# Kernel tuning notes

Hardware: AMD Instinct MI355X
Metric: run time of the kernel (lower is better)

## Reference

```python
import jax, jax.numpy as jnp
import numpy as np

V, BLK, D, H, L = 50257, 2048, 768, 12, 4
HD = D // H
EPS = 1e-5


def _ln(x, w, b):
    mu = jnp.mean(x, axis=-1, keepdims=True)
    var = jnp.mean(jnp.square(x - mu), axis=-1, keepdims=True)
    return (x - mu) * jax.lax.rsqrt(var + EPS) * w + b


def setup_inputs() -> dict:
    key = jax.random.key(0)
    ks = iter(jax.random.split(key, 32))
    s = 0.02
    idx = jax.random.randint(next(ks), (2, 2048), 0, V)
    inp = {
        "idx": idx,
        "wte": jax.random.normal(next(ks), (V, D), jnp.float32) * s,
        "wpe": jax.random.normal(next(ks), (BLK, D), jnp.float32) * s,
        # stacked per-layer params [L, ...]
        "ln1_w": jnp.ones((L, D), jnp.float32),
        "ln1_b": jnp.zeros((L, D), jnp.float32),
        "attn_w": jax.random.normal(next(ks), (L, D, 3 * D), jnp.float32) * s,
        "attn_b": jnp.zeros((L, 3 * D), jnp.float32),
        "proj_w": jax.random.normal(next(ks), (L, D, D), jnp.float32) * (s / np.sqrt(2 * L)),
        "proj_b": jnp.zeros((L, D), jnp.float32),
        "ln2_w": jnp.ones((L, D), jnp.float32),
        "ln2_b": jnp.zeros((L, D), jnp.float32),
        "fc_w": jax.random.normal(next(ks), (L, D, 4 * D), jnp.float32) * s,
        "fc_b": jnp.zeros((L, 4 * D), jnp.float32),
        "fcp_w": jax.random.normal(next(ks), (L, 4 * D, D), jnp.float32) * (s / np.sqrt(2 * L)),
        "fcp_b": jnp.zeros((L, D), jnp.float32),
        "lnf_w": jnp.ones((D,), jnp.float32),
        "lnf_b": jnp.zeros((D,), jnp.float32),
    }
    return inp


def _gpt_forward(idx, wte, wpe, ln1_w, ln1_b, attn_w, attn_b, proj_w, proj_b,
                 ln2_w, ln2_b, fc_w, fc_b, fcp_w, fcp_b, lnf_w, lnf_b):
    B, T = idx.shape
    x = wte[idx] + wpe[:T]  # [B,T,D]; dropout p=0 -> identity
    causal = jnp.tril(jnp.ones((T, T), bool))
    scale = 1.0 / np.sqrt(HD)

    def block(x, p):
        l1w, l1b, aw, ab, pw, pb, l2w, l2b, fw, fb, fpw, fpb = p
        h = _ln(x, l1w, l1b)
        qkv = h @ aw + ab  # [B,T,3D]
        q, k, v = jnp.split(qkv, 3, axis=-1)
        q = q.reshape(B, T, H, HD).transpose(0, 2, 1, 3)  # [B,H,T,hd]
        k = k.reshape(B, T, H, HD).transpose(0, 2, 1, 3)
        v = v.reshape(B, T, H, HD).transpose(0, 2, 1, 3)
        att = jnp.einsum('bhqd,bhkd->bhqk', q, k) * scale
        att = jnp.where(causal, att, -jnp.inf)
        att = jax.nn.softmax(att, axis=-1)
        y = jnp.einsum('bhqk,bhkd->bhqd', att, v)
        y = y.transpose(0, 2, 1, 3).reshape(B, T, D)
        x = x + y @ pw + pb
        h2 = _ln(x, l2w, l2b)
        m = jax.nn.gelu(h2 @ fw + fb, approximate=False) @ fpw + fpb
        return x + m, None

    params = (ln1_w, ln1_b, attn_w, attn_b, proj_w, proj_b,
              ln2_w, ln2_b, fc_w, fc_b, fcp_w, fcp_b)
    x, _ = jax.lax.scan(block, x, params)
    x = _ln(x, lnf_w, lnf_b)
    # inference path: logits only for last position, lm_head tied to wte
    logits = x[:, -1:, :] @ wte.T  # [B,1,V]
    return logits


def reference(idx, wte, wpe, ln1_w, ln1_b, attn_w, attn_b, proj_w, proj_b,
              ln2_w, ln2_b, fc_w, fc_b, fcp_w, fcp_b, lnf_w, lnf_b):
    return _gpt_forward(idx, wte, wpe, ln1_w, ln1_b, attn_w, attn_b, proj_w, proj_b,
                        ln2_w, ln2_b, fc_w, fc_b, fcp_w, fcp_b, lnf_w, lnf_b)
```

## Files before the change

kernel.cpp:

```cpp
#include <hip/hip_runtime.h>
#include <math.h>

#define V 50257
#define B 2
#define T 2048
#define D 768
#define H 12
#define HD 64
#define L 4
#define D3 (3*D)
#define D4 (4*D)
#define NTOK (B*T)
#define EPS 1e-5f

typedef __bf16 v8bf __attribute__((ext_vector_type(8)));
typedef __bf16 v4bf __attribute__((ext_vector_type(4)));
typedef unsigned short v8us __attribute__((ext_vector_type(8)));
typedef float  v4f  __attribute__((ext_vector_type(4)));

#define GAS(p) ((const __attribute__((address_space(1))) void*)(p))
#define LAS(p) ((__attribute__((address_space(3))) void*)(p))

#define LIDX(row, chunk) ((row)*64 + ((((chunk) ^ ((row)&7)))<<3))
#define CIDX(row, chunk) ((row)*128 + ((((chunk) ^ ((row)&7)))<<3))

#define SBAR() asm volatile("s_barrier" ::: "memory")

__global__ __launch_bounds__(256) void prep_kernel(
        const int* __restrict__ idx, const float* __restrict__ wte,
        const float* __restrict__ wpe, float* __restrict__ x,
        const float* __restrict__ aw_all,  const float* __restrict__ pw_all,
        const float* __restrict__ fw_all,  const float* __restrict__ fpw_all,
        __bf16* __restrict__ awt_all, __bf16* __restrict__ pwt_all,
        __bf16* __restrict__ fwt_all, __bf16* __restrict__ fpwt_all) {
    int bid = blockIdx.x;
    if (bid < 3072) {
        int e = (bid * 256 + threadIdx.x) * 4;
        int pos = e / D;
        int d   = e - pos * D;
        int t   = pos & (T - 1);
        int tok = idx[pos];
        const float4 a  = *(const float4*)(wte + (size_t)tok * D + d);
        const float4 p4 = *(const float4*)(wpe + (size_t)t * D + d);
        float4 r; r.x = a.x + p4.x; r.y = a.y + p4.y; r.z = a.z + p4.z; r.w = a.w + p4.w;
        *(float4*)(x + e) = r;
        return;
    }
    bid -= 3072;
    const int l = bid / 6912; bid -= l * 6912;
    const float* W; __bf16* Wt; int K, N, bx, by;
    if (bid < 1728)      {             W = aw_all  + (size_t)l * D  * D3; Wt = awt_all  + (size_t)l * D3 * D;  K = D;  N = D3; bx = bid % 72; by = bid / 72; }
    else if (bid < 2304) { bid -= 1728; W = pw_all  + (size_t)l * D  * D;  Wt = pwt_all  + (size_t)l * D  * D;  K = D;  N = D;  bx = bid % 24; by = bid / 24; }
    else if (bid < 4608) { bid -= 2304; W = fw_all  + (size_t)l * D  * D4; Wt = fwt_all  + (size_t)l * D4 * D;  K = D;  N = D4; bx = bid % 96; by = bid / 96; }
    else                 { bid -= 4608; W = fpw_all + (size_t)l * D4 * D;  Wt = fpwt_all + (size_t)l * D  * D4; K = D4; N = D;  bx = bid % 24; by = bid / 24; }
    __shared__ float t[32][33];
    const int n0 = bx * 32, k0 = by * 32;
    const int tx = threadIdx.x & 31, ty = threadIdx.x >> 5;
    #pragma unroll
    for (int p = 0; p < 4; ++p)
        t[ty + 8 * p][tx] = W[(size_t)(k0 + ty + 8 * p) * N + n0 + tx];
    __syncthreads();
    #pragma unroll
    for (int p = 0; p < 4; ++p)
        Wt[(size_t)(n0 + ty + 8 * p) * K + k0 + tx] = (__bf16)t[tx][ty + 8 * p];
}

__global__ __launch_bounds__(256) void ln_kernel(const float* __restrict__ X,
                                                 const float* __restrict__ w,
                                                 const float* __restrict__ b,
                                                 __bf16* __restrict__ Y,
                                                 int src_mul, int src_off) {
    int srow = blockIdx.x * src_mul + src_off;
    const float* xr = X + (size_t)srow * D;
    float v[3];
    float s = 0.f, s2 = 0.f;
    #pragma unroll
    for (int j = 0; j < 3; ++j) {
        v[j] = xr[threadIdx.x + 256 * j];
        s += v[j];
        s2 += v[j] * v[j];
    }
    #pragma unroll
    for (int off = 32; off; off >>= 1) {
        s  += __shfl_xor(s, off);
        s2 += __shfl_xor(s2, off);
    }
    __shared__ float ss[4], ss2[4];
    int wave = threadIdx.x >> 6, lane = threadIdx.x & 63;
    if (lane == 0) { ss[wave] = s; ss2[wave] = s2; }
    __syncthreads();
    s  = ss[0] + ss[1] + ss[2] + ss[3];
    s2 = ss2[0] + ss2[1] + ss2[2] + ss2[3];
    float mu  = s * (1.f / D);
    float var = s2 * (1.f / D) - mu * mu;
    float rs  = rsqrtf(var + EPS);
    __bf16* yr = Y + (size_t)blockIdx.x * D;
    #pragma unroll
    for (int j = 0; j < 3; ++j) {
        int c = threadIdx.x + 256 * j;
        yr[c] = (__bf16)((v[j] - mu) * rs * w[c] + b[c]);
    }
}

template<bool DOGELU>
__global__ __launch_bounds__(256) void gemm_bt(const __bf16* __restrict__ A,
                                               const __bf16* __restrict__ Wt,
                                               const float* __restrict__ bias,
                                               __bf16* __restrict__ Cout,
                                               int N, int K) {
    __shared__ __align__(16) __bf16 sm[24576];
    const int tid  = threadIdx.x;
    const int w    = tid >> 6;
    const int lane = tid & 63;

    int fid = blockIdx.y * gridDim.x + blockIdx.x;
    const int nwg = gridDim.x * gridDim.y;
    fid = (fid & 7) * (nwg >> 3) + (fid >> 3);
    const int row0 = (fid / gridDim.x) * 128;
    const int col0 = (fid % gridDim.x) * 128;

    const int srow = ((tid >> 6) & 3) * 16 + (tid & 15);
    const int sk   = ((tid >> 4) & 3) * 8;
    const __bf16* gA0 = A  + (size_t)(row0 + srow) * K + sk;
    const __bf16* gA1 = gA0 + (size_t)64 * K;
    const __bf16* gB0 = Wt + (size_t)(col0 + srow) * K + sk;
    const __bf16* gB1 = gB0 + (size_t)64 * K;

    auto stage = [&](int bsel) {
        __bf16* dst = sm + bsel * 8192;
        __builtin_amdgcn_global_load_lds(GAS(gA0), LAS(dst + (size_t)tid * 8), 16, 0, 0);
        __builtin_amdgcn_global_load_lds(GAS(gA1), LAS(dst + (size_t)(tid + 256) * 8), 16, 0, 0);
        __builtin_amdgcn_global_load_lds(GAS(gB0), LAS(dst + 4096 + (size_t)tid * 8), 16, 0, 0);
        __builtin_amdgcn_global_load_lds(GAS(gB1), LAS(dst + 4096 + (size_t)(tid + 256) * 8), 16, 0, 0);
        gA0 += 32; gA1 += 32; gB0 += 32; gB1 += 32;
    };

    const int wr = w >> 1, wc = w & 1;
    const __bf16* rA = sm + wr * 2048 + lane * 8;
    const __bf16* rB = sm + 4096 + wc * 2048 + lane * 8;

    const int nt = K >> 5;
    stage(0); stage(1);

    v4f acc[4][4] = {};
    for (int t = 0; t < nt; ++t) {
        const int cb = (t % 3) * 8192;
        if (t + 2 < nt) {
            stage((t + 2) % 3);
            asm volatile("s_waitcnt vmcnt(8)\n\ts_barrier" ::: "memory");
        } else if (t + 1 < nt) {
            asm volatile("s_waitcnt vmcnt(4)\n\ts_barrier" ::: "memory");
        } else {
            asm volatile("s_waitcnt vmcnt(0)\n\ts_barrier" ::: "memory");
        }
        v8bf af[4], bfr[4];
        #pragma unroll
        for (int i = 0; i < 4; ++i) af[i]  = *(const v8bf*)(rA + cb + i * 512);
        #pragma unroll
        for (int j = 0; j < 4; ++j) bfr[j] = *(const v8bf*)(rB + cb + j * 512);
        #pragma unroll
        for (int i = 0; i < 4; ++i)
            #pragma unroll
            for (int j = 0; j < 4; ++j)
                acc[i][j] = __builtin_amdgcn_mfma_f32_16x16x32_bf16(af[i], bfr[j], acc[i][j], 0, 0, 0);
        SBAR();
    }

    const int er = (lane >> 4) * 4;
    const int ec = lane & 15;
    #pragma unroll
    for (int j = 0; j < 4; ++j) {
        const int col = wc * 64 + j * 16 + ec;
        const float bval = bias[col0 + col];
        const int chunk = col >> 3, ce = col & 7;
        #pragma unroll
        for (int i = 0; i < 4; ++i) {
            const int rowb = wr * 64 + i * 16 + er;
            #pragma unroll
            for (int rr = 0; rr < 4; ++rr) {
                float vv = acc[i][j][rr] + bval;
                if (DOGELU) vv = 0.5f * vv * (1.f + erff(vv * 0.70710678118f));
                sm[CIDX(rowb + rr, chunk) + ce] = (__bf16)vv;
            }
        }
    }
    __syncthreads();
    #pragma unroll
    for (int c = 0; c < 8; ++c) {
        const int chunkid = tid + c * 256;
        const int row = chunkid >> 4;
        const int cc  = chunkid & 15;
        *(v8us*)(void*)(Cout + (size_t)(row0 + row) * N + col0 + cc * 8) =
            *(const v8us*)(const void*)(sm + CIDX(row, cc));
    }
}

__global__ __launch_bounds__(256) void gemm64(const __bf16* __restrict__ A,
                                              const __bf16* __restrict__ Wt,
                                              const float* __restrict__ bias,
                                              const float* __restrict__ res,
                                              float* __restrict__ Cout,
                                              int N, int K) {
    __shared__ __align__(16) __bf16 sm[24576];
    const int tid  = threadIdx.x;
    const int w    = tid >> 6;
    const int lane = tid & 63;

    int fid = blockIdx.y * gridDim.x + blockIdx.x;
    const int nwg = gridDim.x * gridDim.y;
    fid = (fid & 7) * (nwg >> 3) + (fid >> 3);
    const int row0 = (fid / gridDim.x) * 64;
    const int col0 = (fid % gridDim.x) * 64;

    const int srow = ((tid >> 7) & 3) * 16 + (tid & 15);
    const int sk   = ((tid >> 4) & 7) * 8;
    const __bf16* gA0 = A  + (size_t)(row0 + srow) * K + sk;
    const __bf16* gA1 = gA0 + (size_t)32 * K;
    const __bf16* gB0 = Wt + (size_t)(col0 + srow) * K + sk;
    const __bf16* gB1 = gB0 + (size_t)32 * K;

    auto stage = [&](int bsel) {
        __bf16* dst = sm + bsel * 8192;
        __builtin_amdgcn_global_load_lds(GAS(gA0), LAS(dst + (size_t)tid * 8), 16, 0, 0);
        __builtin_amdgcn_global_load_lds(GAS(gA1), LAS(dst + (size_t)(tid + 256) * 8), 16, 0, 0);
        __builtin_amdgcn_global_load_lds(GAS(gB0), LAS(dst + 4096 + (size_t)tid * 8), 16, 0, 0);
        __builtin_amdgcn_global_load_lds(GAS(gB1), LAS(dst + 4096 + (size_t)(tid + 256) * 8), 16, 0, 0);
        gA0 += 64; gA1 += 64; gB0 += 64; gB1 += 64;
    };

    const int wr = w >> 1, wc = w & 1;
    const __bf16* rA = sm + wr * 2048 + lane * 8;
    const __bf16* rB = sm + 4096 + wc * 2048 + lane * 8;

    const int nt = K >> 6;
    stage(0); stage(1);

    v4f acc[2][2] = {};
    for (int t = 0; t < nt; ++t) {
        const int cb = (t % 3) * 8192;
        if (t + 2 < nt) {
            stage((t + 2) % 3);
            asm volatile("s_waitcnt vmcnt(8)\n\ts_barrier" ::: "memory");
        } else if (t + 1 < nt) {
            asm volatile("s_waitcnt vmcnt(4)\n\ts_barrier" ::: "memory");
        } else {
            asm volatile("s_waitcnt vmcnt(0)\n\ts_barrier" ::: "memory");
        }
        #pragma unroll
        for (int h = 0; h < 2; ++h) {
            v8bf af[2], bfr[2];
            #pragma unroll
            for (int i = 0; i < 2; ++i) af[i]  = *(const v8bf*)(rA + cb + i * 1024 + h * 512);
            #pragma unroll
            for (int j = 0; j < 2; ++j) bfr[j] = *(const v8bf*)(rB + cb + j * 1024 + h * 512);
            #pragma unroll
            for (int i = 0; i < 2; ++i)
                #pragma unroll
                for (int j = 0; j < 2; ++j)
                    acc[i][j] = __builtin_amdgcn_mfma_f32_16x16x32_bf16(af[i], bfr[j], acc[i][j], 0, 0, 0);
        }
        SBAR();
    }

    float* smf = (float*)sm;
    const int er = (lane >> 4) * 4;
    const int ec = lane & 15;
    #pragma unroll
    for (int j = 0; j < 2; ++j) {
        const int col = wc * 32 + j * 16 + ec;
        const float bval = bias[col0 + col];
        #pragma unroll
        for (int i = 0; i < 2; ++i) {
            #pragma unroll
            for (int rr = 0; rr < 4; ++rr) {
                const int row = wr * 32 + i * 16 + er + rr;
                smf[row * 64 + (col ^ ((row & 3) << 4))] = acc[i][j][rr] + bval;
            }
        }
    }
    __syncthreads();
    #pragma unroll
    for (int c = 0; c < 4; ++c) {
        const int chunkid = tid + c * 256;
        const int row = chunkid >> 4;
        const int c0  = (chunkid & 15) * 4;
        float4 vv = *(const float4*)(smf + row * 64 + (c0 ^ ((row & 3) << 4)));
        const float4 rv = *(const float4*)(res + (size_t)(row0 + row) * N + col0 + c0);
        vv.x += rv.x; vv.y += rv.y; vv.z += rv.z; vv.w += rv.w;
        *(float4*)(Cout + (size_t)(row0 + row) * N + col0 + c0) = vv;
    }
}

__global__ __launch_bounds__(256) void attn_mfma(const __bf16* __restrict__ qkv,
                                                 __bf16* __restrict__ y) {
    __shared__ __align__(16) __bf16 Qs[4096];
    __shared__ __align__(16) __bf16 Ks[4096];
    __shared__ __align__(16) __bf16 Vt[4096];
    __shared__ __align__(16) __bf16 Ps[4][1024];

    const int tid  = threadIdx.x;
    const int w    = tid >> 6;
    const int lane = tid & 63;
    const int quad = lane >> 4;
    const int l4   = lane & 15;

    int fid = blockIdx.x;
    const int nwg = gridDim.x;
    fid = (fid & 7) * (nwg >> 3) + (fid >> 3);

    const int qt = 31 - (fid & 31);
    const int bh = fid >> 5;
    const int b  = bh / H;
    const int h  = bh - b * H;
    const int q0 = qt * 64;

    const __bf16* base = qkv + (size_t)(b * T) * D3 + h * HD;

    {
        int c = tid;
        #pragma unroll
        for (int rep = 0; rep < 2; ++rep, c += 256) {
            int row = c >> 3, ch = c & 7;
            v8us v = *(const v8us*)(const void*)(base + (size_t)(q0 + row) * D3 + ch * 8);
            *(v8us*)(void*)(Qs + LIDX(row, ch)) = v;
        }
    }

    const int krow = tid >> 3, kch = tid & 7;
    const int vkp = tid & 31, vdc = tid >> 5;
    const __bf16* kp0 = base + D     + (size_t)krow * D3 + kch * 8;
    const __bf16* kp1 = kp0 + (size_t)32 * D3;
    const __bf16* vp0 = base + 2 * D + (size_t)(2 * vkp) * D3 + vdc * 8;
    const __bf16* vp1 = vp0 + D3;

    v8us kr0 = *(const v8us*)(const void*)kp0;
    v8us kr1 = *(const v8us*)(const void*)kp1;
    v8us vr0 = *(const v8us*)(const void*)vp0;
    v8us vr1 = *(const v8us*)(const void*)vp1;

    float m_local = -INFINITY;
    v4f o[4] = {};
    v4f sacc = {};
    v8bf qf[2];
    v8bf vones;
    #pragma unroll
    for (int i = 0; i < 8; ++i) vones[i] = (__bf16)1.0f;

    const int nt = qt + 1;
    const size_t adv = (size_t)64 * D3;
    const int qrow = q0 + w * 16 + l4;

    for (int kt = 0; kt < nt; ++kt) {
        const int k0 = kt * 64;
        *(v8us*)(void*)(Ks + LIDX(krow, kch))      = kr0;
        *(v8us*)(void*)(Ks + LIDX(krow + 32, kch)) = kr1;
        #pragma unroll
        for (int j = 0; j < 8; ++j) {
            int dim = vdc * 8 + j;
            int idx = dim * 64 + ((((vkp >> 2) ^ (dim & 7))) << 3) + ((vkp & 3) << 1);
            *(unsigned int*)(void*)(Vt + idx) =
                ((unsigned int)vr1[j] << 16) | (unsigned int)vr0[j];
        }
        __syncthreads();

        if (kt == 0) {
            #pragma unroll
            for (int kh = 0; kh < 2; ++kh)
                qf[kh] = *(const v8bf*)(Qs + LIDX(w * 16 + l4, kh * 4 + quad));
        }
        if (kt + 1 < nt) {
            kp0 += adv; kp1 += adv; vp0 += adv; vp1 += adv;
            kr0 = *(const v8us*)(const void*)kp0;
            kr1 = *(const v8us*)(const void*)kp1;
            vr0 = *(const v8us*)(const void*)vp0;
            vr1 = *(const v8us*)(const void*)vp1;
        }

        v4f s[4] = {};
        __builtin_amdgcn_s_setprio(1);
        #pragma unroll
        for (int kh = 0; kh < 2; ++kh) {
            #pragma unroll
            for (int jb = 0; jb < 4; ++jb) {
                v8bf bk = *(const v8bf*)(Ks + LIDX(jb * 16 + l4, kh * 4 + quad));
                s[jb] = __builtin_amdgcn_mfma_f32_16x16x32_bf16(bk, qf[kh], s[jb], 0, 0, 0);
            }
        }
        __builtin_amdgcn_s_setprio(0);

        float sv[4][4];
        float mx = -INFINITY;
        #pragma unroll
        for (int jb = 0; jb < 4; ++jb) {
            #pragma unroll
            for (int rg = 0; rg < 4; ++rg) {
                float vvv = s[jb][rg] * 0.125f;
                if (k0 + jb * 16 + quad * 4 + rg > qrow) vvv = -INFINITY;
                sv[jb][rg] = vvv;
                mx = fmaxf(mx, vvv);
            }
        }
        mx = fmaxf(mx, __shfl_xor(mx, 16));
        mx = fmaxf(mx, __shfl_xor(mx, 32));
        if (!__all(mx <= m_local + 8.f)) {
            const float mnew    = fmaxf(m_local, mx);
            const float alpha_l = __expf(m_local - mnew);
            m_local = mnew;
            float a4[4];
            #pragma unroll
            for (int r = 0; r < 4; ++r) a4[r] = __shfl(alpha_l, quad * 4 + r);
            #pragma unroll
            for (int r = 0; r < 4; ++r) {
                sacc[r] *= a4[r];
                #pragma unroll
                for (int db = 0; db < 4; ++db) o[db][r] *= a4[r];
            }
        }
        #pragma unroll
        for (int jb = 0; jb < 4; ++jb) {
            v4bf pk;
            #pragma unroll
            for (int rg = 0; rg < 4; ++rg)
                pk[rg] = (__bf16)__expf(sv[jb][rg] - m_local);
            *(v4bf*)(void*)(&Ps[w][LIDX(l4, jb * 2 + (quad >> 1)) + ((quad & 1) << 2)]) = pk;
        }
        __builtin_amdgcn_s_setprio(1);
        #pragma unroll
        for (int kh = 0; kh < 2; ++kh) {
            v8bf ap = *(const v8bf*)(&Ps[w][LIDX(l4, kh * 4 + quad)]);
            sacc = __builtin_amdgcn_mfma_f32_16x16x32_bf16(ap, vones, sacc, 0, 0, 0);
            #pragma unroll
            for (int db = 0; db < 4; ++db) {
                v8bf bv = *(const v8bf*)(Vt + LIDX(db * 16 + l4, kh * 4 + quad));
                o[db] = __builtin_amdgcn_mfma_f32_16x16x32_bf16(ap, bv, o[db], 0, 0, 0);
            }
        }
        __builtin_amdgcn_s_setprio(0);
        __syncthreads();
    }

    #pragma unroll
    for (int db = 0; db < 4; ++db) {
        #pragma unroll
        for (int r = 0; r < 4; ++r) {
            const int q = q0 + w * 16 + quad * 4 + r;
            y[(size_t)(b * T + q) * D + h * HD + db * 16 + l4] =
                (__bf16)(o[db][r] / sacc[r]);
        }
    }
}

__global__ __launch_bounds__(256) void logits_kernel(const __bf16* __restrict__ xf,
                                                     const float* __restrict__ wte,
                                                     float* __restrict__ out) {
    int wave = threadIdx.x >> 6;
    int lane = threadIdx.x & 63;
    int v = blockIdx.x * 4 + wave;
    if (v >= V) return;
    const float4* wr = (const float4*)(wte + (size_t)v * D);
    const v4bf*   x0 = (const v4bf*)(xf);
    const v4bf*   x1 = (const v4bf*)(xf + D);
    float s0 = 0.f, s1 = 0.f;
    #pragma unroll
    for (int j = 0; j < 3; ++j) {
        float4 wv = wr[lane + 64 * j];
        v4bf a0 = x0[lane + 64 * j];
        v4bf a1 = x1[lane + 64 * j];
        s0 = fmaf(wv.x, (float)a0[0], s0); s0 = fmaf(wv.y, (float)a0[1], s0);
        s0 = fmaf(wv.z, (float)a0[2], s0); s0 = fmaf(wv.w, (float)a0[3], s0);
        s1 = fmaf(wv.x, (float)a1[0], s1); s1 = fmaf(wv.y, (float)a1[1], s1);
        s1 = fmaf(wv.z, (float)a1[2], s1); s1 = fmaf(wv.w, (float)a1[3], s1);
    }
    #pragma unroll
    for (int off = 32; off; off >>= 1) {
        s0 += __shfl_xor(s0, off);
        s1 += __shfl_xor(s1, off);
    }
    if (lane == 0) { out[v] = s0; out[V + v] = s1; }
}

extern "C" void kernel_launch(void* const* d_in, const int* in_sizes, int n_in,
                              void* d_out, int out_size, void* d_ws, size_t ws_size,
                              hipStream_t stream) {
    const int*   idx    = (const int*)  d_in[0];
    const float* wte    = (const float*)d_in[1];
    const float* wpe    = (const float*)d_in[2];
    const float* ln1_w  = (const float*)d_in[3];
    const float* ln1_b  = (const float*)d_in[4];
    const float* attn_w = (const float*)d_in[5];
    const float* attn_b = (const float*)d_in[6];
    const float* proj_w = (const float*)d_in[7];
    const float* proj_b = (const float*)d_in[8];
    const float* ln2_w  = (const float*)d_in[9];
    const float* ln2_b  = (const float*)d_in[10];
    const float* fc_w   = (const float*)d_in[11];
    const float* fc_b   = (const float*)d_in[12];
    const float* fcp_w  = (const float*)d_in[13];
    const float* fcp_b  = (const float*)d_in[14];
    const float* lnf_w  = (const float*)d_in[15];
    const float* lnf_b  = (const float*)d_in[16];
    float* out = (float*)d_out;

    char* ws = (char*)d_ws;
    float*  x    = (float*)ws;  ws += (size_t)NTOK * D  * 4;
    __bf16* qkvb = (__bf16*)ws;
    __bf16* gb   = (__bf16*)ws; ws += (size_t)NTOK * D4 * 2;
    __bf16* hb   = (__bf16*)ws; ws += (size_t)NTOK * D  * 2;
    __bf16* yb   = (__bf16*)ws; ws += (size_t)NTOK * D  * 2;
    __bf16* awt  = (__bf16*)ws; ws += (size_t)L * D3 * D   * 2;
    __bf16* pwt  = (__bf16*)ws; ws += (size_t)L * D  * D   * 2;
    __bf16* fwt  = (__bf16*)ws; ws += (size_t)L * D4 * D   * 2;
    __bf16* fpwt = (__bf16*)ws; ws += (size_t)L * D  * D4  * 2;
    __bf16* xf   = (__bf16*)ws; ws += (size_t)B * D    * 2;

    prep_kernel<<<3072 + 6912 * L, 256, 0, stream>>>(idx, wte, wpe, x,
                                                     attn_w, proj_w, fc_w, fcp_w,
                                                     awt, pwt, fwt, fpwt);

    for (int l = 0; l < L; ++l) {
        const float* l1w = ln1_w + l * D;
        const float* l1b = ln1_b + l * D;
        const float* ab  = attn_b + l * D3;
        const float* pb  = proj_b + l * D;
        const float* l2w = ln2_w + l * D;
        const float* l2b = ln2_b + l * D;
        const float* fb  = fc_b + l * D4;
        const float* fpb = fcp_b + l * D;
        const __bf16* awl  = awt  + (size_t)l * D3 * D;
        const __bf16* pwl  = pwt  + (size_t)l * D  * D;
        const __bf16* fwl  = fwt  + (size_t)l * D4 * D;
        const __bf16* fpwl = fpwt + (size_t)l * D  * D4;

        ln_kernel<<<NTOK, 256, 0, stream>>>(x, l1w, l1b, hb, 1, 0);
        gemm_bt<false><<<dim3(D3 / 128, NTOK / 128), 256, 0, stream>>>(
            hb, awl, ab, qkvb, D3, D);
        attn_mfma<<<B * H * (T / 64), 256, 0, stream>>>(qkvb, yb);
        gemm64<<<dim3(D / 64, NTOK / 64), 256, 0, stream>>>(
            yb, pwl, pb, x, x, D, D);
        ln_kernel<<<NTOK, 256, 0, stream>>>(x, l2w, l2b, hb, 1, 0);
        gemm_bt<true><<<dim3(D4 / 128, NTOK / 128), 256, 0, stream>>>(
            hb, fwl, fb, gb, D4, D);
        gemm64<<<dim3(D / 64, NTOK / 64), 256, 0, stream>>>(
            gb, fpwl, fpb, x, x, D, D4);
    }

    ln_kernel<<<B, 256, 0, stream>>>(x, lnf_w, lnf_b, xf, T, T - 1);
    logits_kernel<<<(V + 3) / 4, 256, 0, stream>>>(xf, wte, out);
}
```

Measured before the change: 1.265 ms.

## Double-buffer K/V tiles in attention and use polynomial erf for GELU

The attention kernel now keeps two LDS buffers for the K and V tiles, so it writes the next tile while the current one is consumed, and it needs one barrier per iteration instead of two. The goal is to overlap LDS staging with the MFMA and softmax work and to cut synchronization. The FC GELU epilogue also swaps erff for an Abramowitz-Stegun polynomial erf approximation with about 1e-7 error, which lowers epilogue ALU cost at a small accuracy risk. LDS use rises by 16 KB per block, which may reduce occupancy.

Result: no change. 1.251 ms (-1.1%).

```diff
diff --git a/kernel.cpp b/kernel.cpp
--- a/kernel.cpp
+++ b/kernel.cpp
@@ -25,6 +25,16 @@
 #define CIDX(row, chunk) ((row)*128 + ((((chunk) ^ ((row)&7)))<<3))
 
 #define SBAR() asm volatile("s_barrier" ::: "memory")
+
+__device__ __forceinline__ float gelu_fast(float x) {
+    float z  = fabsf(x) * 0.70710678118f;
+    float tt = 1.f / (1.f + 0.3275911f * z);
+    float poly = tt * (0.254829592f + tt * (-0.284496736f + tt * (1.421413741f +
+                 tt * (-1.453152027f + tt * 1.061405429f))));
+    float er = 1.f - poly * __expf(-z * z);
+    er = (x < 0.f) ? -er : er;
+    return 0.5f * x * (1.f + er);
+}
 
 __global__ __launch_bounds__(256) void prep_kernel(
         const int* __restrict__ idx, const float* __restrict__ wte,
@@ -179,7 +189,7 @@
             #pragma unroll
             for (int rr = 0; rr < 4; ++rr) {
                 float vv = acc[i][j][rr] + bval;
-                if (DOGELU) vv = 0.5f * vv * (1.f + erff(vv * 0.70710678118f));
+                if (DOGELU) vv = gelu_fast(vv);
                 sm[CIDX(rowb + rr, chunk) + ce] = (__bf16)vv;
             }
         }
@@ -294,8 +304,8 @@
 __global__ __launch_bounds__(256) void attn_mfma(const __bf16* __restrict__ qkv,
                                                  __bf16* __restrict__ y) {
     __shared__ __align__(16) __bf16 Qs[4096];
-    __shared__ __align__(16) __bf16 Ks[4096];
-    __shared__ __align__(16) __bf16 Vt[4096];
+    __shared__ __align__(16) __bf16 Ks[8192];
+    __shared__ __align__(16) __bf16 Vt[8192];
     __shared__ __align__(16) __bf16 Ps[4][1024];
 
     const int tid  = threadIdx.x;
@@ -338,43 +348,45 @@
     v8us vr0 = *(const v8us*)(const void*)vp0;
     v8us vr1 = *(const v8us*)(const void*)vp1;
 
+    const int nt = qt + 1;
+    const size_t adv = (size_t)64 * D3;
+
+    *(v8us*)(void*)(Ks + LIDX(krow, kch))      = kr0;
+    *(v8us*)(void*)(Ks + LIDX(krow + 32, kch)) = kr1;
+    #pragma unroll
+    for (int j = 0; j < 8; ++j) {
+        int dim = vdc * 8 + j;
+        int idx = dim * 64 + ((((vkp >> 2) ^ (dim & 7))) << 3) + ((vkp & 3) << 1);
+        *(unsigned int*)(void*)(Vt + idx) =
+            ((unsigned int)vr1[j] << 16) | (unsigned int)vr0[j];
+    }
+    if (nt > 1) {
+        kp0 += adv; kp1 += adv; vp0 += adv; vp1 += adv;
+        kr0 = *(const v8us*)(const void*)kp0;
+        kr1 = *(const v8us*)(const void*)kp1;
+        vr0 = *(const v8us*)(const void*)vp0;
+        vr1 = *(const v8us*)(const void*)vp1;
+    }
+    __syncthreads();
+
+    v8bf qf[2];
+    #pragma unroll
+    for (int kh = 0; kh < 2; ++kh)
+        qf[kh] = *(const v8bf*)(Qs + LIDX(w * 16 + l4, kh * 4 + quad));
+
     float m_local = -INFINITY;
     v4f o[4] = {};
     v4f sacc = {};
-    v8bf qf[2];
     v8bf vones;
     #pragma unroll
     for (int i = 0; i < 8; ++i) vones[i] = (__bf16)1.0f;
 
-    const int nt = qt + 1;
-    const size_t adv = (size_t)64 * D3;
     const int qrow = q0 + w * 16 + l4;
 
     for (int kt = 0; kt < nt; ++kt) {
+        const int cur = (kt & 1) << 12;
+        const int nxt = cur ^ 4096;
         const int k0 = kt * 64;
-        *(v8us*)(void*)(Ks + LIDX(krow, kch))      = kr0;
-        *(v8us*)(void*)(Ks + LIDX(krow + 32, kch)) = kr1;
-        #pragma unroll
-        for (int j = 0; j < 8; ++j) {
-            int dim = vdc * 8 + j;
-            int idx = dim * 64 + ((((vkp >> 2) ^ (dim & 7))) << 3) + ((vkp & 3) << 1);
-            *(unsigned int*)(void*)(Vt + idx) =
-                ((unsigned int)vr1[j] << 16) | (unsigned int)vr0[j];
-        }
-        __syncthreads();
-
-        if (kt == 0) {
-            #pragma unroll
-            for (int kh = 0; kh < 2; ++kh)
-                qf[kh] = *(const v8bf*)(Qs + LIDX(w * 16 + l4, kh * 4 + quad));
-        }
-        if (kt + 1 < nt) {
-            kp0 += adv; kp1 += adv; vp0 += adv; vp1 += adv;
-            kr0 = *(const v8us*)(const void*)kp0;
-            kr1 = *(const v8us*)(const void*)kp1;
-            vr0 = *(const v8us*)(const void*)vp0;
-            vr1 = *(const v8us*)(const void*)vp1;
-        }
 
         v4f s[4] = {};
         __builtin_amdgcn_s_setprio(1);
@@ -382,11 +394,30 @@
         for (int kh = 0; kh < 2; ++kh) {
             #pragma unroll
             for (int jb = 0; jb < 4; ++jb) {
-                v8bf bk = *(const v8bf*)(Ks + LIDX(jb * 16 + l4, kh * 4 + quad));
+                v8bf bk = *(const v8bf*)(Ks + cur + LIDX(jb * 16 + l4, kh * 4 + quad));
                 s[jb] = __builtin_amdgcn_mfma_f32_16x16x32_bf16(bk, qf[kh], s[jb], 0, 0, 0);
             }
         }
         __builtin_amdgcn_s_setprio(0);
+
+        if (kt + 1 < nt) {
+            *(v8us*)(void*)(Ks + nxt + LIDX(krow, kch))      = kr0;
+            *(v8us*)(void*)(Ks + nxt + LIDX(krow + 32, kch)) = kr1;
+            #pragma unroll
+            for (int j = 0; j < 8; ++j) {
+                int dim = vdc * 8 + j;
+                int idx = dim * 64 + ((((vkp >> 2) ^ (dim & 7))) << 3) + ((vkp & 3) << 1);
+                *(unsigned int*)(void*)(Vt + nxt + idx) =
+                    ((unsigned int)vr1[j] << 16) | (unsigned int)vr0[j];
+            }
+            if (kt + 2 < nt) {
+                kp0 += adv; kp1 += adv; vp0 += adv; vp1 += adv;
+                kr0 = *(const v8us*)(const void*)kp0;
+                kr1 = *(const v8us*)(const void*)kp1;
+                vr0 = *(const v8us*)(const void*)vp0;
+                vr1 = *(const v8us*)(const void*)vp1;
+            }
+        }
 
         float sv[4][4];
         float mx = -INFINITY;
@@ -431,12 +462,12 @@
             sacc = __builtin_amdgcn_mfma_f32_16x16x32_bf16(ap, vones, sacc, 0, 0, 0);
             #pragma unroll
             for (int db = 0; db < 4; ++db) {
-                v8bf bv = *(const v8bf*)(Vt + LIDX(db * 16 + l4, kh * 4 + quad));
+                v8bf bv = *(const v8bf*)(Vt + cur + LIDX(db * 16 + l4, kh * 4 + quad));
                 o[db] = __builtin_amdgcn_mfma_f32_16x16x32_bf16(ap, bv, o[db], 0, 0, 0);
             }
         }
         __builtin_amdgcn_s_setprio(0);
-        __syncthreads();
+        if (kt + 1 < nt) __syncthreads();
     }
 
     #pragma unroll
```
